# Kernel optimization log

Hardware: AMD Instinct MI355X
Metric: run time of the kernel (lower is better)

The kernel has to match this reference:

```python
import jax, jax.numpy as jnp
import numpy as np
import math

D_MODEL, D_FF, N_EXPERTS, TOP_K, N_SHARED = 1024, 4096, 8, 2, 1
B, T = 4, 1024
SCALE = 1.0 / math.sqrt(N_SHARED + TOP_K / N_EXPERTS)


def setup_inputs() -> dict:
    key = jax.random.key(0)
    ks = jax.random.split(key, 10)
    s1 = 1.0 / math.sqrt(D_MODEL)
    s2 = 1.0 / math.sqrt(D_FF)
    return {
        "x": jax.random.normal(ks[0], (B, T, D_MODEL), dtype=jnp.float32),
        "w_router": jax.random.normal(ks[1], (N_EXPERTS, D_MODEL), dtype=jnp.float32) * s1,
        "W1": jax.random.normal(ks[2], (N_EXPERTS, D_FF, D_MODEL), dtype=jnp.float32) * s1,
        "b1": jax.random.normal(ks[3], (N_EXPERTS, D_FF), dtype=jnp.float32) * 0.02,
        "W2": jax.random.normal(ks[4], (N_EXPERTS, D_MODEL, D_FF), dtype=jnp.float32) * s2,
        "b2": jax.random.normal(ks[5], (N_EXPERTS, D_MODEL), dtype=jnp.float32) * 0.02,
        "Ws1": jax.random.normal(ks[6], (D_FF, D_MODEL), dtype=jnp.float32) * s1,
        "bs1": jax.random.normal(ks[7], (D_FF,), dtype=jnp.float32) * 0.02,
        "Ws2": jax.random.normal(ks[8], (D_MODEL, D_FF), dtype=jnp.float32) * s2,
        "bs2": jax.random.normal(ks[9], (D_MODEL,), dtype=jnp.float32) * 0.02,
    }


def reference(x, w_router, W1, b1, W2, b2, Ws1, bs1, Ws2, bs2):
    # Router: logits -> softmax -> top-k gate values (no renormalization, matching source)
    logits = jnp.einsum("btd,ed->bte", x, w_router)      # [B,T,E]
    probs = jax.nn.softmax(logits, axis=-1)
    vals, idx = jax.lax.top_k(probs, TOP_K)               # [B,T,K]
    # Scatter top-k gate values into dense per-expert gates [B,T,E]
    gates = jnp.sum(jax.nn.one_hot(idx, N_EXPERTS, dtype=x.dtype) * vals[..., None], axis=-2)

    # Shared (always-on) expert FFN
    hs = jax.nn.gelu(jnp.einsum("btd,fd->btf", x, Ws1) + bs1)
    acc = jnp.einsum("btf,df->btd", hs, Ws2) + bs2

    # Routed experts, densified combine: sum_e gate[b,t,e] * FFN_e(x[b,t])
    h = jax.nn.gelu(jnp.einsum("btd,efd->btef", x, W1) + b1)   # [B,T,E,F]
    y = jnp.einsum("btef,edf->bted", h, W2) + b2               # [B,T,E,D]
    acc = acc + jnp.einsum("bted,bte->btd", y, gates)

    return SCALE * acc
```

## Files before the change

kernel.cpp:

```cpp
#include <hip/hip_runtime.h>
#include <hip/hip_bf16.h>

#define NTOK 4096
#define DM   1024
#define DF   4096
#define ROWS_TOTAL 12288
#define BM 128
#define BN 128
#define BK 64
#define SCALE_F 0.8944271909999159f
#define PMAX 103

typedef __attribute__((ext_vector_type(8))) short short8;
typedef __attribute__((ext_vector_type(4))) float floatx4;

#define GLD16(gp, lp) __builtin_amdgcn_global_load_lds( \
    (const __attribute__((address_space(1))) void*)(gp), \
    (__attribute__((address_space(3))) void*)(lp), 16, 0, 0)

__device__ __forceinline__ ushort f2bf(float f){
    __hip_bfloat16 h = __float2bfloat16(f);
    return *reinterpret_cast<ushort*>(&h);
}

__device__ __forceinline__ float gelu_tanh(float v){
    float u2 = -1.5957691216057308f * (v + 0.044715f * v * v * v);
    return v / (1.0f + __expf(u2));
}

#define CVT_N0 1048576u
#define CVT_N1 9437184u
#define CVT_N2 17825792u
#define CVT_N3 18874368u
#define CVT_N4 19922944u
__global__ __launch_bounds__(256) void cvt_all(
    const float* __restrict__ x,  const float* __restrict__ W1,
    const float* __restrict__ W2, const float* __restrict__ Ws1,
    const float* __restrict__ Ws2,
    ushort* __restrict__ xb,  ushort* __restrict__ w1b, ushort* __restrict__ w2b,
    ushort* __restrict__ ws1b, ushort* __restrict__ ws2b)
{
    unsigned i = blockIdx.x * 256u + threadIdx.x;
    const float* s; ushort* d; unsigned off;
    if      (i < CVT_N0){ s = x;   d = xb;   off = i; }
    else if (i < CVT_N1){ s = W1;  d = w1b;  off = i - CVT_N0; }
    else if (i < CVT_N2){ s = W2;  d = w2b;  off = i - CVT_N1; }
    else if (i < CVT_N3){ s = Ws1; d = ws1b; off = i - CVT_N2; }
    else                { s = Ws2; d = ws2b; off = i - CVT_N3; }
    float4 v = reinterpret_cast<const float4*>(s)[off];
    ushort4 o = { f2bf(v.x), f2bf(v.y), f2bf(v.z), f2bf(v.w) };
    reinterpret_cast<ushort4*>(d)[off] = o;
}

__global__ __launch_bounds__(256) void router_kernel(
    const float* __restrict__ x, const float* __restrict__ wr,
    int* __restrict__ te, float* __restrict__ tg, int* __restrict__ tokarr)
{
    const int token = blockIdx.x * 4 + (threadIdx.x >> 6);
    const int lane  = threadIdx.x & 63;
    const float* xp = x + (size_t)token * DM;
    float s[8];
    #pragma unroll
    for (int e = 0; e < 8; e++) s[e] = 0.f;
    for (int d = lane; d < DM; d += 64){
        float xv = xp[d];
        #pragma unroll
        for (int e = 0; e < 8; e++) s[e] += xv * wr[e * DM + d];
    }
    #pragma unroll
    for (int e = 0; e < 8; e++){
        float v = s[e];
        #pragma unroll
        for (int off = 32; off > 0; off >>= 1) v += __shfl_down(v, off);
        s[e] = v;
    }
    if (lane == 0){
        float m = s[0];
        #pragma unroll
        for (int e = 1; e < 8; e++) m = fmaxf(m, s[e]);
        float p[8]; float sum = 0.f;
        #pragma unroll
        for (int e = 0; e < 8; e++){ p[e] = __expf(s[e] - m); sum += p[e]; }
        float inv = 1.f / sum;
        #pragma unroll
        for (int e = 0; e < 8; e++) p[e] *= inv;
        int i1 = 0; float p1 = p[0];
        #pragma unroll
        for (int e = 1; e < 8; e++) if (p[e] > p1){ p1 = p[e]; i1 = e; }
        int i2 = -1; float p2 = -1.f;
        #pragma unroll
        for (int e = 0; e < 8; e++) if (e != i1 && p[e] > p2){ p2 = p[e]; i2 = e; }
        te[token*2+0] = i1; te[token*2+1] = i2;
        tg[token*2+0] = p1; tg[token*2+1] = p2;
        tokarr[token] = token;
    }
}

__global__ __launch_bounds__(256) void plan_kernel(
    const int* __restrict__ te, int* __restrict__ tokarr,
    int* __restrict__ rowof, int* __restrict__ meta)
{
    __shared__ int lc[9], lcur[9];
    const int t = threadIdx.x;
    if (t < 9) lc[t] = 0;
    __syncthreads();
    for (int j = t; j < NTOK*2; j += 256) atomicAdd(&lc[te[j]], 1);
    __syncthreads();
    if (t == 0){
        int off = NTOK;
        for (int e = 0; e < 8; e++){
            lcur[e]    = off;
            meta[e]    = lc[e];
            meta[16+e] = off;
            meta[32+e] = (lc[e] + BM - 1) / BM;
            off += lc[e];
        }
        meta[8]    = NTOK;
        meta[16+8] = 0;
        meta[32+8] = NTOK / BM;
    }
    __syncthreads();
    for (int j = t; j < NTOK*2; j += 256){
        int e = te[j];
        int p = atomicAdd(&lcur[e], 1);
        tokarr[p] = j >> 1;
        rowof[j]  = p;
    }
}

template<int MODE>
__global__ __launch_bounds__(256) void gemm_kernel(
    const ushort* __restrict__ Abase,
    const ushort* __restrict__ Wb, const ushort* __restrict__ Wsb,
    const float* __restrict__ brout, const float* __restrict__ bsh,
    const int* __restrict__ meta, const int* __restrict__ tokarr,
    ushort* __restrict__ Hout, float* __restrict__ Yout)
{
    const int xcd = blockIdx.x & 7;
    const int q   = blockIdx.x >> 3;
    const int NTG = (MODE == 0) ? 4 : 1;

    int e = -1, r = 0, a0 = 0;
    #pragma unroll
    for (int ee = 0; ee < 9; ee++){
        int w = NTG * meta[32 + ee];
        if (e < 0 && q < a0 + w){ e = ee; r = q - a0; }
        a0 += w;
    }
    if (e < 0) return;
    const int mt_e = meta[32 + e];
    int ntg, mti;
    if (MODE == 0){ ntg = r / mt_e; mti = r - ntg * mt_e; }
    else          { ntg = 0;        mti = r; }
    const int nt   = (MODE == 0) ? (xcd + 8 * ntg) : xcd;
    const int cnt  = meta[e];
    const int base = meta[16 + e];

    const int K = (MODE == 0) ? DM : DF;
    const int N = (MODE == 0) ? DF : DM;
    const ushort* Bp  = (e < 8) ? (Wb + (size_t)e * DF * DM) : Wsb;
    const float* bias = (e < 8) ? (brout + e * N) : bsh;

    __shared__ ushort As[BM * BK];
    __shared__ ushort Bs[BN * BK];

    const int t    = threadIdx.x;
    const int lane = t & 63;
    const int wv   = t >> 6;
    const int wm   = (wv >> 1) * 64;
    const int wn   = (wv & 1) * 64;
    const int lrow = lane & 15;
    const int quad = lane >> 4;
    const int swz8 = ((lane & 7) ^ (lane >> 3)) * 8;

    const ushort* Ap[4];
    const ushort* Bpp[4];
    ushort* Alds[4];
    ushort* Blds[4];
    #pragma unroll
    for (int i = 0; i < 4; i++){
        int rin = wv * 32 + i * 8 + (lane >> 3);
        int pos = mti * BM + rin;
        int clp = (pos < cnt) ? pos : (cnt - 1);
        if (MODE == 0) Ap[i] = Abase + (size_t)tokarr[base + clp] * DM + swz8;
        else           Ap[i] = Abase + (size_t)(base + clp) * DF + swz8;
        Bpp[i]  = Bp + (size_t)(nt * BN + rin) * K + swz8;
        Alds[i] = &As[(wv * 32 + i * 8) * BK];
        Blds[i] = &Bs[(wv * 32 + i * 8) * BK];
    }

    floatx4 acc[4][4];
    #pragma unroll
    for (int mi = 0; mi < 4; mi++)
        #pragma unroll
        for (int ni = 0; ni < 4; ni++)
            acc[mi][ni] = (floatx4){0.f, 0.f, 0.f, 0.f};

    for (int k0 = 0; k0 < K; k0 += BK){
        __syncthreads();
        #pragma unroll
        for (int i = 0; i < 4; i++){
            GLD16(Ap[i]  + k0, Alds[i]);
            GLD16(Bpp[i] + k0, Blds[i]);
        }
        __syncthreads();
        #pragma unroll
        for (int kk = 0; kk < BK; kk += 32){
            short8 af[4], bfr[4];
            #pragma unroll
            for (int mi = 0; mi < 4; mi++){
                int row  = wm + mi * 16 + lrow;
                int phys = ((kk >> 3) + quad) ^ (row & 7);
                af[mi] = *reinterpret_cast<const short8*>(&As[row * BK + phys * 8]);
            }
            #pragma unroll
            for (int ni = 0; ni < 4; ni++){
                int row  = wn + ni * 16 + lrow;
                int phys = ((kk >> 3) + quad) ^ (row & 7);
                bfr[ni] = *reinterpret_cast<const short8*>(&Bs[row * BK + phys * 8]);
            }
            #pragma unroll
            for (int mi = 0; mi < 4; mi++)
                #pragma unroll
                for (int ni = 0; ni < 4; ni++)
                    acc[mi][ni] = __builtin_amdgcn_mfma_f32_16x16x32_bf16(af[mi], bfr[ni], acc[mi][ni], 0, 0, 0);
        }
    }

    float bv[4];
    #pragma unroll
    for (int ni = 0; ni < 4; ni++) bv[ni] = bias[nt * BN + wn + ni*16 + lrow];

    #pragma unroll
    for (int mi = 0; mi < 4; mi++){
        #pragma unroll
        for (int rg = 0; rg < 4; rg++){
            int s   = wm + mi*16 + quad*4 + rg;
            int pos = mti * BM + s;
            if (pos >= cnt) continue;
            int rr = base + pos;
            if (MODE == 0){
                ushort* hp = Hout + (size_t)rr * DF + nt * BN;
                #pragma unroll
                for (int ni = 0; ni < 4; ni++){
                    float v = acc[mi][ni][rg] + bv[ni];
                    hp[wn + ni*16 + lrow] = f2bf(gelu_tanh(v));
                }
            } else {
                float* yp = Yout + (size_t)rr * DM + nt * BN;
                #pragma unroll
                for (int ni = 0; ni < 4; ni++)
                    yp[wn + ni*16 + lrow] = acc[mi][ni][rg] + bv[ni];
            }
        }
    }
}

__global__ __launch_bounds__(256) void combine_kernel(
    const float* __restrict__ Y, const int* __restrict__ rowof,
    const float* __restrict__ tg, float* __restrict__ out)
{
    const int token = blockIdx.x;
    const int d4    = threadIdx.x;
    const float4* Y4 = reinterpret_cast<const float4*>(Y);
    int r1 = rowof[token*2+0], r2 = rowof[token*2+1];
    float g1 = tg[token*2+0],  g2 = tg[token*2+1];
    float4 a = Y4[(size_t)token * 256 + d4];
    float4 b = Y4[(size_t)r1 * 256 + d4];
    float4 c = Y4[(size_t)r2 * 256 + d4];
    float4 o;
    o.x = SCALE_F * (a.x + g1*b.x + g2*c.x);
    o.y = SCALE_F * (a.y + g1*b.y + g2*c.y);
    o.z = SCALE_F * (a.z + g1*b.z + g2*c.z);
    o.w = SCALE_F * (a.w + g1*b.w + g2*c.w);
    reinterpret_cast<float4*>(out)[(size_t)token * 256 + d4] = o;
}

extern "C" void kernel_launch(void* const* d_in, const int* in_sizes, int n_in,
                              void* d_out, int out_size, void* d_ws, size_t ws_size,
                              hipStream_t stream) {
    const float* x   = (const float*)d_in[0];
    const float* wr  = (const float*)d_in[1];
    const float* W1  = (const float*)d_in[2];
    const float* b1  = (const float*)d_in[3];
    const float* W2  = (const float*)d_in[4];
    const float* b2  = (const float*)d_in[5];
    const float* Ws1 = (const float*)d_in[6];
    const float* bs1 = (const float*)d_in[7];
    const float* Ws2 = (const float*)d_in[8];
    const float* bs2 = (const float*)d_in[9];
    float* out = (float*)d_out;

    char* ws = (char*)d_ws;
    size_t off = 0;
    auto wsalloc = [&](size_t bytes) -> char* {
        char* p = ws + off;
        off += (bytes + 255) & ~(size_t)255;
        return p;
    };
    ushort* xb   = (ushort*)wsalloc((size_t)NTOK * DM * 2);
    ushort* w1b  = (ushort*)wsalloc((size_t)8 * DF * DM * 2);
    ushort* w2b  = (ushort*)wsalloc((size_t)8 * DM * DF * 2);
    ushort* ws1b = (ushort*)wsalloc((size_t)DF * DM * 2);
    ushort* ws2b = (ushort*)wsalloc((size_t)DM * DF * 2);
    ushort* H    = (ushort*)wsalloc((size_t)ROWS_TOTAL * DF * 2);
    int*    tokarr = (int*)wsalloc(ROWS_TOTAL * 4);
    int*    rowof  = (int*)wsalloc(NTOK * 2 * 4);
    int*    te     = (int*)wsalloc(NTOK * 2 * 4);
    float*  tg     = (float*)wsalloc(NTOK * 2 * 4);
    int*    meta   = (int*)wsalloc(64 * 4);
    float*  Y = (float*)w1b;

    cvt_all<<<CVT_N4/256, 256, 0, stream>>>(x, W1, W2, Ws1, Ws2,
                                            xb, w1b, w2b, ws1b, ws2b);
    router_kernel<<<NTOK/4, 256, 0, stream>>>(x, wr, te, tg, tokarr);
    plan_kernel<<<1, 256, 0, stream>>>(te, tokarr, rowof, meta);

    gemm_kernel<0><<<8 * 4 * PMAX, 256, 0, stream>>>(xb, w1b, ws1b, b1, bs1,
        meta, tokarr, H, Y);
    gemm_kernel<1><<<8 * PMAX, 256, 0, stream>>>(H, w2b, ws2b, b2, bs2,
        meta, tokarr, H, Y);

    combine_kernel<<<NTOK, 256, 0, stream>>>(Y, rowof, tg, out);
}
```

Before: 722.1 us.

## Drop weight bf16 pre-conversion; load fp32 weights and convert in GEMM

Removes the separate cvt_all pass that turned all expert and shared weights into bf16. The GEMMs now stage fp32 weight tiles into LDS with a swizzled layout and convert them to bf16 while building MFMA fragments. The x-to-bf16 cast moves into the router kernel, and the plan kernel swaps shared-memory atomics for ballot/popcount ranking. This saves the large weight read/write pass but doubles B-tile LDS footprint and global traffic inside the GEMMs and adds per-fragment conversion ALU work.

```diff
diff --git a/kernel.cpp b/kernel.cpp
--- a/kernel.cpp
+++ b/kernel.cpp
@@ -28,33 +28,10 @@
     return v / (1.0f + __expf(u2));
 }
 
-#define CVT_N0 1048576u
-#define CVT_N1 9437184u
-#define CVT_N2 17825792u
-#define CVT_N3 18874368u
-#define CVT_N4 19922944u
-__global__ __launch_bounds__(256) void cvt_all(
-    const float* __restrict__ x,  const float* __restrict__ W1,
-    const float* __restrict__ W2, const float* __restrict__ Ws1,
-    const float* __restrict__ Ws2,
-    ushort* __restrict__ xb,  ushort* __restrict__ w1b, ushort* __restrict__ w2b,
-    ushort* __restrict__ ws1b, ushort* __restrict__ ws2b)
-{
-    unsigned i = blockIdx.x * 256u + threadIdx.x;
-    const float* s; ushort* d; unsigned off;
-    if      (i < CVT_N0){ s = x;   d = xb;   off = i; }
-    else if (i < CVT_N1){ s = W1;  d = w1b;  off = i - CVT_N0; }
-    else if (i < CVT_N2){ s = W2;  d = w2b;  off = i - CVT_N1; }
-    else if (i < CVT_N3){ s = Ws1; d = ws1b; off = i - CVT_N2; }
-    else                { s = Ws2; d = ws2b; off = i - CVT_N3; }
-    float4 v = reinterpret_cast<const float4*>(s)[off];
-    ushort4 o = { f2bf(v.x), f2bf(v.y), f2bf(v.z), f2bf(v.w) };
-    reinterpret_cast<ushort4*>(d)[off] = o;
-}
-
 __global__ __launch_bounds__(256) void router_kernel(
     const float* __restrict__ x, const float* __restrict__ wr,
-    int* __restrict__ te, float* __restrict__ tg, int* __restrict__ tokarr)
+    int* __restrict__ te, float* __restrict__ tg, int* __restrict__ tokarr,
+    ushort* __restrict__ xb)
 {
     const int token = blockIdx.x * 4 + (threadIdx.x >> 6);
     const int lane  = threadIdx.x & 63;
@@ -64,6 +41,7 @@
     for (int e = 0; e < 8; e++) s[e] = 0.f;
     for (int d = lane; d < DM; d += 64){
         float xv = xp[d];
+        xb[(size_t)token * DM + d] = f2bf(xv);
         #pragma unroll
         for (int e = 0; e < 8; e++) s[e] += xv * wr[e * DM + d];
     }
@@ -100,29 +78,55 @@
     const int* __restrict__ te, int* __restrict__ tokarr,
     int* __restrict__ rowof, int* __restrict__ meta)
 {
-    __shared__ int lc[9], lcur[9];
+    __shared__ int wcnt[4][32][8];
+    __shared__ int ebase[8];
     const int t = threadIdx.x;
-    if (t < 9) lc[t] = 0;
+    const int w = t >> 6, l = t & 63;
+    for (int r = 0; r < 32; r++){
+        int e = te[w*2048 + r*64 + l];
+        #pragma unroll
+        for (int ee = 0; ee < 8; ee++){
+            unsigned long long m = __ballot(e == ee);
+            if (l == 0) wcnt[w][r][ee] = __popcll(m);
+        }
+    }
     __syncthreads();
-    for (int j = t; j < NTOK*2; j += 256) atomicAdd(&lc[te[j]], 1);
+    if (t < 8){
+        int run = 0;
+        for (int w2 = 0; w2 < 4; w2++)
+            for (int r = 0; r < 32; r++){
+                int v = wcnt[w2][r][t];
+                wcnt[w2][r][t] = run;
+                run += v;
+            }
+        ebase[t] = run;
+    }
     __syncthreads();
     if (t == 0){
         int off = NTOK;
         for (int e = 0; e < 8; e++){
-            lcur[e]    = off;
-            meta[e]    = lc[e];
+            int c = ebase[e];
+            meta[e]    = c;
             meta[16+e] = off;
-            meta[32+e] = (lc[e] + BM - 1) / BM;
-            off += lc[e];
+            meta[32+e] = (c + BM - 1) / BM;
+            ebase[e]   = off;
+            off += c;
         }
         meta[8]    = NTOK;
         meta[16+8] = 0;
         meta[32+8] = NTOK / BM;
     }
     __syncthreads();
-    for (int j = t; j < NTOK*2; j += 256){
+    for (int r = 0; r < 32; r++){
+        int j = w*2048 + r*64 + l;
         int e = te[j];
-        int p = atomicAdd(&lcur[e], 1);
+        int rank = 0;
+        #pragma unroll
+        for (int ee = 0; ee < 8; ee++){
+            unsigned long long m = __ballot(e == ee);
+            if (e == ee) rank = __popcll(m & ((1ull << l) - 1ull));
+        }
+        int p = ebase[e] + wcnt[w][r][e] + rank;
         tokarr[p] = j >> 1;
         rowof[j]  = p;
     }
@@ -131,7 +135,7 @@
 template<int MODE>
 __global__ __launch_bounds__(256) void gemm_kernel(
     const ushort* __restrict__ Abase,
-    const ushort* __restrict__ Wb, const ushort* __restrict__ Wsb,
+    const float* __restrict__ Wb, const float* __restrict__ Wsb,
     const float* __restrict__ brout, const float* __restrict__ bsh,
     const int* __restrict__ meta, const int* __restrict__ tokarr,
     ushort* __restrict__ Hout, float* __restrict__ Yout)
@@ -158,11 +162,11 @@
 
     const int K = (MODE == 0) ? DM : DF;
     const int N = (MODE == 0) ? DF : DM;
-    const ushort* Bp  = (e < 8) ? (Wb + (size_t)e * DF * DM) : Wsb;
+    const float* Bp   = (e < 8) ? (Wb + (size_t)e * DF * DM) : Wsb;
     const float* bias = (e < 8) ? (brout + e * N) : bsh;
 
     __shared__ ushort As[BM * BK];
-    __shared__ ushort Bs[BN * BK];
+    __shared__ float  Bsf[BN * BK];
 
     const int t    = threadIdx.x;
     const int lane = t & 63;
@@ -171,22 +175,27 @@
     const int wn   = (wv & 1) * 64;
     const int lrow = lane & 15;
     const int quad = lane >> 4;
-    const int swz8 = ((lane & 7) ^ (lane >> 3)) * 8;
 
     const ushort* Ap[4];
-    const ushort* Bpp[4];
     ushort* Alds[4];
-    ushort* Blds[4];
+    const int aswz = ((lane & 7) ^ (lane >> 3)) * 8;
     #pragma unroll
     for (int i = 0; i < 4; i++){
         int rin = wv * 32 + i * 8 + (lane >> 3);
         int pos = mti * BM + rin;
         int clp = (pos < cnt) ? pos : (cnt - 1);
-        if (MODE == 0) Ap[i] = Abase + (size_t)tokarr[base + clp] * DM + swz8;
-        else           Ap[i] = Abase + (size_t)(base + clp) * DF + swz8;
-        Bpp[i]  = Bp + (size_t)(nt * BN + rin) * K + swz8;
+        if (MODE == 0) Ap[i] = Abase + (size_t)tokarr[base + clp] * DM + aswz;
+        else           Ap[i] = Abase + (size_t)(base + clp) * DF + aswz;
         Alds[i] = &As[(wv * 32 + i * 8) * BK];
-        Blds[i] = &Bs[(wv * 32 + i * 8) * BK];
+    }
+    const float* Bpp[8];
+    float* Blds[8];
+    #pragma unroll
+    for (int i = 0; i < 8; i++){
+        int rin = wv * 32 + i * 4 + (lane >> 4);
+        int sgl = (lane & 15) ^ (rin & 7);
+        Bpp[i]  = Bp + (size_t)(nt * BN + rin) * K + sgl * 4;
+        Blds[i] = &Bsf[(wv * 32 + i * 4) * BK];
     }
 
     floatx4 acc[4][4];
@@ -196,13 +205,14 @@
         for (int ni = 0; ni < 4; ni++)
             acc[mi][ni] = (floatx4){0.f, 0.f, 0.f, 0.f};
 
+    const float4* Bs4 = reinterpret_cast<const float4*>(Bsf);
+
     for (int k0 = 0; k0 < K; k0 += BK){
         __syncthreads();
         #pragma unroll
-        for (int i = 0; i < 4; i++){
-            GLD16(Ap[i]  + k0, Alds[i]);
-            GLD16(Bpp[i] + k0, Blds[i]);
-        }
+        for (int i = 0; i < 4; i++) GLD16(Ap[i] + k0, Alds[i]);
+        #pragma unroll
+        for (int i = 0; i < 8; i++) GLD16(Bpp[i] + k0, Blds[i]);
         __syncthreads();
         #pragma unroll
         for (int kk = 0; kk < BK; kk += 32){
@@ -215,9 +225,16 @@
             }
             #pragma unroll
             for (int ni = 0; ni < 4; ni++){
-                int row  = wn + ni * 16 + lrow;
-                int phys = ((kk >> 3) + quad) ^ (row & 7);
-                bfr[ni] = *reinterpret_cast<const short8*>(&Bs[row * BK + phys * 8]);
+                int row = wn + ni * 16 + lrow;
+                int kw0 = (kk >> 2) + quad * 2;
+                float4 d0 = Bs4[row * 16 + (kw0      ^ (row & 7))];
+                float4 d1 = Bs4[row * 16 + ((kw0 + 1) ^ (row & 7))];
+                short8 b;
+                b[0] = (short)f2bf(d0.x); b[1] = (short)f2bf(d0.y);
+                b[2] = (short)f2bf(d0.z); b[3] = (short)f2bf(d0.w);
+                b[4] = (short)f2bf(d1.x); b[5] = (short)f2bf(d1.y);
+                b[6] = (short)f2bf(d1.z); b[7] = (short)f2bf(d1.w);
+                bfr[ni] = b;
             }
             #pragma unroll
             for (int mi = 0; mi < 4; mi++)
@@ -299,26 +316,20 @@
         return p;
     };
     ushort* xb   = (ushort*)wsalloc((size_t)NTOK * DM * 2);
-    ushort* w1b  = (ushort*)wsalloc((size_t)8 * DF * DM * 2);
-    ushort* w2b  = (ushort*)wsalloc((size_t)8 * DM * DF * 2);
-    ushort* ws1b = (ushort*)wsalloc((size_t)DF * DM * 2);
-    ushort* ws2b = (ushort*)wsalloc((size_t)DM * DF * 2);
     ushort* H    = (ushort*)wsalloc((size_t)ROWS_TOTAL * DF * 2);
+    float*  Y    = (float*) wsalloc((size_t)ROWS_TOTAL * DM * 4);
     int*    tokarr = (int*)wsalloc(ROWS_TOTAL * 4);
     int*    rowof  = (int*)wsalloc(NTOK * 2 * 4);
     int*    te     = (int*)wsalloc(NTOK * 2 * 4);
     float*  tg     = (float*)wsalloc(NTOK * 2 * 4);
     int*    meta   = (int*)wsalloc(64 * 4);
-    float*  Y = (float*)w1b;
-
-    cvt_all<<<CVT_N4/256, 256, 0, stream>>>(x, W1, W2, Ws1, Ws2,
-                                            xb, w1b, w2b, ws1b, ws2b);
-    router_kernel<<<NTOK/4, 256, 0, stream>>>(x, wr, te, tg, tokarr);
+
+    router_kernel<<<NTOK/4, 256, 0, stream>>>(x, wr, te, tg, tokarr, xb);
     plan_kernel<<<1, 256, 0, stream>>>(te, tokarr, rowof, meta);
 
-    gemm_kernel<0><<<8 * 4 * PMAX, 256, 0, stream>>>(xb, w1b, ws1b, b1, bs1,
+    gemm_kernel<0><<<8 * 4 * PMAX, 256, 0, stream>>>(xb, W1, Ws1, b1, bs1,
         meta, tokarr, H, Y);
-    gemm_kernel<1><<<8 * PMAX, 256, 0, stream>>>(H, w2b, ws2b, b2, bs2,
+    gemm_kernel<1><<<8 * PMAX, 256, 0, stream>>>(H, W2, Ws2, b2, bs2,
         meta, tokarr, H, Y);
 
     combine_kernel<<<NTOK, 256, 0, stream>>>(Y, rowof, tg, out);
```

Measured after the change: 748.7 us. 3.7% more time.
